# Performance work log

Measured on AMD Instinct MI355X. Metric: run time of the kernel, lower is better.

Reference implementation:

```python
import jax, jax.numpy as jnp
import numpy as np

N_NODES = 100000
N_EDGES = 1600000
NFEAT, NHID, NCLASS = 512, 256, 128
K_HOPS = 5
ALPHA = 0.1


def setup_inputs() -> dict:
    key = jax.random.key(0)
    ks = jax.random.split(key, 7)
    x = jax.random.normal(ks[0], (N_NODES, NFEAT), dtype=jnp.float32)
    edge_index = jax.random.randint(ks[1], (2, N_EDGES), 0, N_NODES, dtype=jnp.int64)
    edge_weight = jax.random.uniform(ks[2], (N_EDGES,), dtype=jnp.float32)
    # Glorot-ish scaled linear weights
    W1 = jax.random.normal(ks[3], (NFEAT, NHID), dtype=jnp.float32) * (1.0 / np.sqrt(NFEAT))
    b1 = jnp.zeros((NHID,), dtype=jnp.float32)
    W2 = jax.random.normal(ks[4], (NHID, NCLASS), dtype=jnp.float32) * (1.0 / np.sqrt(NHID))
    b2 = jnp.zeros((NCLASS,), dtype=jnp.float32)
    return {"x": x, "edge_index": edge_index, "edge_weight": edge_weight,
            "W1": W1, "b1": b1, "W2": W2, "b2": b2}


def reference(x, edge_index, edge_weight, W1, b1, W2, b2):
    # 2-layer MLP (act after first layer only; dropout p=0)
    h = jnp.maximum(x @ W1 + b1, 0.0)
    h = h @ W2 + b2  # [N, nclass]
    src = edge_index[0]
    dst = edge_index[1]
    x0 = h

    def step(carry, _):
        # gather by source, scale by edge weight, scatter-add at target
        msg = carry[src] * edge_weight[:, None]          # [E, nclass]
        agg = jax.ops.segment_sum(msg, dst, num_segments=N_NODES)
        out = (1.0 - ALPHA) * agg + ALPHA * x0           # restart mix
        return out, None

    xK, _ = jax.lax.scan(step, x0, None, length=K_HOPS)
    return jax.nn.log_softmax(xK, axis=1)
```

## Files before the change

kernel.cpp:

```cpp
#include <hip/hip_runtime.h>
#include <hip/hip_bf16.h>
#include <cstdint>
#include <cstddef>

#define N_NODES 100000
#define NFEAT 512
#define NHID 256
#define NCLASS 128
#define K_HOPS 5
#define ALPHA 0.1f

typedef __attribute__((ext_vector_type(8))) short short8v;
typedef __attribute__((ext_vector_type(4))) float f32x4;

__device__ __forceinline__ unsigned short f2bf(float f) {
    unsigned u = __builtin_bit_cast(unsigned, f);
    u += 0x7FFFu + ((u >> 16) & 1u);
    return (unsigned short)(u >> 16);
}
__device__ __forceinline__ float bflo(unsigned u) {
    return __builtin_bit_cast(float, u << 16);
}
__device__ __forceinline__ float bfhi(unsigned u) {
    return __builtin_bit_cast(float, u & 0xFFFF0000u);
}
__device__ __forceinline__ unsigned cvtpk2(float a, float b) {
    unsigned r;
    asm("v_cvt_pk_bf16_f32 %0, %1, %2" : "=v"(r) : "v"(a), "v"(b));
    return r;
}
__device__ __forceinline__ void gload_lds16(const void* g, void* l) {
    __builtin_amdgcn_global_load_lds((const __attribute__((address_space(1))) void*)g,
                                     (__attribute__((address_space(3))) void*)l, 16, 0, 0);
}


__global__ void count_kernel(const int* __restrict__ dst, int* __restrict__ counts, int E) {
    int i = blockIdx.x * blockDim.x + threadIdx.x;
    if (i < E) atomicAdd(&counts[dst[i]], 1);
}

__global__ __launch_bounds__(256) void scan_p1(const int* __restrict__ counts,
                                               int* __restrict__ partial, int n) {
    __shared__ int ws[4];
    int b = blockIdx.x, t = threadIdx.x;
    int base = b * 1024 + t * 4;
    int s = 0;
#pragma unroll
    for (int j = 0; j < 4; ++j) {
        int idx = base + j;
        if (idx < n) s += counts[idx];
    }
#pragma unroll
    for (int off = 32; off; off >>= 1) s += __shfl_xor(s, off, 64);
    if ((t & 63) == 0) ws[t >> 6] = s;
    __syncthreads();
    if (t == 0) partial[b] = ws[0] + ws[1] + ws[2] + ws[3];
}

__global__ __launch_bounds__(128) void scan_p2(int* __restrict__ partial, int nb) {
    __shared__ int s[128];
    int t = threadIdx.x;
    int v = (t < nb) ? partial[t] : 0;
    s[t] = v;
    __syncthreads();
    for (int off = 1; off < 128; off <<= 1) {
        int u = (t >= off) ? s[t - off] : 0;
        __syncthreads();
        s[t] += u;
        __syncthreads();
    }
    if (t < nb) partial[t] = (t == 0) ? 0 : s[t - 1];
}

__global__ __launch_bounds__(256) void scan_p3(const int* __restrict__ counts,
                                               const int* __restrict__ partial,
                                               int* __restrict__ row_ptr,
                                               int* __restrict__ fill, int n) {
    __shared__ int ts[256];
    int b = blockIdx.x, t = threadIdx.x;
    int base = b * 1024 + t * 4;
    int c[4];
#pragma unroll
    for (int j = 0; j < 4; ++j) {
        int idx = base + j;
        c[j] = (idx < n) ? counts[idx] : 0;
    }
    int s = c[0] + c[1] + c[2] + c[3];
    ts[t] = s;
    __syncthreads();
    for (int off = 1; off < 256; off <<= 1) {
        int v = (t >= off) ? ts[t - off] : 0;
        __syncthreads();
        ts[t] += v;
        __syncthreads();
    }
    int pre = partial[b] + ((t == 0) ? 0 : ts[t - 1]);
#pragma unroll
    for (int j = 0; j < 4; ++j) {
        int idx = base + j;
        if (idx < n) {
            row_ptr[idx] = pre;
            fill[idx] = pre;
            if (idx == n - 1) row_ptr[n] = pre + c[j];
            pre += c[j];
        }
    }
}

__global__ void scatter_kernel(const int* __restrict__ src, const int* __restrict__ dst,
                               const float* __restrict__ w, int* __restrict__ fill,
                               int2* __restrict__ epk, int E) {
    int i = blockIdx.x * blockDim.x + threadIdx.x;
    if (i < E) {
        int d = dst[i];
        int pos = atomicAdd(&fill[d], 1);
        int2 m; m.x = src[i]; m.y = __builtin_bit_cast(int, w[i]);
        epk[pos] = m;
    }
}

__global__ void wtrans_kernel(const float* __restrict__ W, unsigned short* __restrict__ Wt,
                              int K, int N) {
    int idx = blockIdx.x * blockDim.x + threadIdx.x;
    if (idx >= N * K) return;
    int n = idx / K, k = idx - n * K;
    Wt[idx] = f2bf(W[(size_t)k * N + n]);
}

template<int K, int N, int RELU, int AF32>
__global__ __launch_bounds__(256) void gemm_mfma(const void* __restrict__ Ain,
                                                 const unsigned short* __restrict__ Wt,
                                                 const float* __restrict__ bias,
                                                 unsigned short* __restrict__ Cout, int M) {
    extern __shared__ char smem[];
    constexpr int ABYTES = AF32 ? 16384 : 8192;
    constexpr int ASTEP  = AF32 ? 128 : 64;
    constexpr int NCA    = AF32 ? 4 : 2;
    char* Abase = smem;
    char* Bbase = smem + 2 * ABYTES;

    const int tid = threadIdx.x;
    const int lane = tid & 63;
    const int wv = tid >> 6;
    const int wr = wv >> 1, wc = wv & 1;
    const int brow = blockIdx.y * 128;
    const int bcol = blockIdx.x * 128;
    const float* Af = (const float*)Ain;
    const unsigned short* Ab = (const unsigned short*)Ain;

    const char* asrc[NCA];
    int aci[NCA];
#pragma unroll
    for (int c = 0; c < NCA; ++c) {
        int ci = wv + c * 4;
        aci[c] = ci;
        int ms = AF32 ? (ci & 7) : ci;
        int koff = (lane >> 4) * 8 + (AF32 ? (ci >> 3) * 4 : 0);
        int ar = brow + ms * 16 + (lane & 15); if (ar > M - 1) ar = M - 1;
        asrc[c] = AF32 ? (const char*)&Af[(size_t)ar * K + koff]
                       : (const char*)&Ab[(size_t)ar * K + koff];
    }
    const char* bsrc[2];
#pragma unroll
    for (int c = 0; c < 2; ++c) {
        int ci = wv + c * 4;
        int bc = bcol + ci * 16 + (lane & 15);
        bsrc[c] = (const char*)&Wt[(size_t)bc * K + (lane >> 4) * 8];
    }

    f32x4 acc[4][4];
#pragma unroll
    for (int m = 0; m < 4; ++m)
#pragma unroll
        for (int n = 0; n < 4; ++n) acc[m][n] = f32x4{0.f, 0.f, 0.f, 0.f};

    auto stage = [&](int buf, int step) {
        char* la = Abase + buf * ABYTES;
        char* lb = Bbase + buf * 8192;
#pragma unroll
        for (int c = 0; c < NCA; ++c)
            gload_lds16(asrc[c] + (size_t)step * ASTEP, la + aci[c] * 1024);
#pragma unroll
        for (int c = 0; c < 2; ++c)
            gload_lds16(bsrc[c] + (size_t)step * 64, lb + (wv + c * 4) * 1024);
    };

    constexpr int NSTEP = K / 32;
    int cur = 0;
    stage(0, 0);
    asm volatile("s_waitcnt vmcnt(0)" ::: "memory");
    __syncthreads();

    for (int s = 0; s < NSTEP; ++s) {
        if (s + 1 < NSTEP) stage(cur ^ 1, s + 1);

        short8v a[4], b[4];
        if constexpr (AF32) {
            const float* Asf = (const float*)(Abase + cur * ABYTES);
#pragma unroll
            for (int m = 0; m < 4; ++m) {
                int g = (wr * 4 + m) * 64 + lane;
                f32x4 lo = *(const f32x4*)&Asf[g * 4];
                f32x4 hi = *(const f32x4*)&Asf[(512 + g) * 4];
                uint4 u;
                u.x = cvtpk2(lo[0], lo[1]); u.y = cvtpk2(lo[2], lo[3]);
                u.z = cvtpk2(hi[0], hi[1]); u.w = cvtpk2(hi[2], hi[3]);
                a[m] = __builtin_bit_cast(short8v, u);
            }
        } else {
            const unsigned short* As16 = (const unsigned short*)(Abase + cur * ABYTES);
#pragma unroll
            for (int m = 0; m < 4; ++m)
                a[m] = *(const short8v*)&As16[((wr * 4 + m) * 64 + lane) * 8];
        }
        const unsigned short* Bs16 = (const unsigned short*)(Bbase + cur * 8192);
#pragma unroll
        for (int n = 0; n < 4; ++n)
            b[n] = *(const short8v*)&Bs16[((wc * 4 + n) * 64 + lane) * 8];

#pragma unroll
        for (int m = 0; m < 4; ++m)
#pragma unroll
            for (int n = 0; n < 4; ++n)
                acc[m][n] = __builtin_amdgcn_mfma_f32_16x16x32_bf16(a[m], b[n], acc[m][n], 0, 0, 0);

        asm volatile("s_waitcnt vmcnt(0)" ::: "memory");
        __syncthreads();
        cur ^= 1;
    }

#pragma unroll
    for (int n = 0; n < 4; ++n) {
        int colg = bcol + wc * 64 + n * 16 + (lane & 15);
        float bv = bias[colg];
#pragma unroll
        for (int m = 0; m < 4; ++m) {
#pragma unroll
            for (int r = 0; r < 4; ++r) {
                int rowg = brow + wr * 64 + m * 16 + (lane >> 4) * 4 + r;
                if (rowg < M) {
                    float v = acc[m][n][r] + bv;
                    if constexpr (RELU) v = fmaxf(v, 0.f);
                    Cout[(size_t)rowg * N + colg] = f2bf(v);
                }
            }
        }
    }
}

template<int FINAL>
__global__ __launch_bounds__(256) void hop_kernel(const unsigned short* __restrict__ carry,
                                                  const unsigned short* __restrict__ c0,
                                                  const int* __restrict__ rp,
                                                  const int2* __restrict__ epk,
                                                  unsigned short* __restrict__ outb,
                                                  float* __restrict__ outf, int nnodes) {
    int node = blockIdx.x * 4 + (threadIdx.x >> 6);
    if (node >= nnodes) return;
    int lane = threadIdx.x & 63;
    int e0 = rp[node], e1 = rp[node + 1];

    float a0x = 0.f, a0y = 0.f, a1x = 0.f, a1y = 0.f;
    float a2x = 0.f, a2y = 0.f, a3x = 0.f, a3y = 0.f;

    for (int eb = e0; eb < e1; eb += 64) {
        int nb = e1 - eb; if (nb > 64) nb = 64;
        int cs = 0, wvi = 0;
        if (lane < nb) {
            int2 m = epk[eb + lane];
            cs = m.x; wvi = m.y;
        }
        int j = 0;
        for (; j + 7 < nb; j += 8) {
            int s0 = __builtin_amdgcn_readlane(cs, j);
            int s1 = __builtin_amdgcn_readlane(cs, j + 1);
            int s2 = __builtin_amdgcn_readlane(cs, j + 2);
            int s3 = __builtin_amdgcn_readlane(cs, j + 3);
            int s4 = __builtin_amdgcn_readlane(cs, j + 4);
            int s5 = __builtin_amdgcn_readlane(cs, j + 5);
            int s6 = __builtin_amdgcn_readlane(cs, j + 6);
            int s7 = __builtin_amdgcn_readlane(cs, j + 7);
            float w0 = __builtin_bit_cast(float, __builtin_amdgcn_readlane(wvi, j));
            float w1 = __builtin_bit_cast(float, __builtin_amdgcn_readlane(wvi, j + 1));
            float w2 = __builtin_bit_cast(float, __builtin_amdgcn_readlane(wvi, j + 2));
            float w3 = __builtin_bit_cast(float, __builtin_amdgcn_readlane(wvi, j + 3));
            float w4 = __builtin_bit_cast(float, __builtin_amdgcn_readlane(wvi, j + 4));
            float w5 = __builtin_bit_cast(float, __builtin_amdgcn_readlane(wvi, j + 5));
            float w6 = __builtin_bit_cast(float, __builtin_amdgcn_readlane(wvi, j + 6));
            float w7 = __builtin_bit_cast(float, __builtin_amdgcn_readlane(wvi, j + 7));
            unsigned u0 = ((const unsigned*)(carry + ((size_t)s0 << 7)))[lane];
            unsigned u1 = ((const unsigned*)(carry + ((size_t)s1 << 7)))[lane];
            unsigned u2 = ((const unsigned*)(carry + ((size_t)s2 << 7)))[lane];
            unsigned u3 = ((const unsigned*)(carry + ((size_t)s3 << 7)))[lane];
            unsigned u4 = ((const unsigned*)(carry + ((size_t)s4 << 7)))[lane];
            unsigned u5 = ((const unsigned*)(carry + ((size_t)s5 << 7)))[lane];
            unsigned u6 = ((const unsigned*)(carry + ((size_t)s6 << 7)))[lane];
            unsigned u7 = ((const unsigned*)(carry + ((size_t)s7 << 7)))[lane];
            a0x = fmaf(w0, bflo(u0), a0x); a0y = fmaf(w0, bfhi(u0), a0y);
            a1x = fmaf(w1, bflo(u1), a1x); a1y = fmaf(w1, bfhi(u1), a1y);
            a2x = fmaf(w2, bflo(u2), a2x); a2y = fmaf(w2, bfhi(u2), a2y);
            a3x = fmaf(w3, bflo(u3), a3x); a3y = fmaf(w3, bfhi(u3), a3y);
            a0x = fmaf(w4, bflo(u4), a0x); a0y = fmaf(w4, bfhi(u4), a0y);
            a1x = fmaf(w5, bflo(u5), a1x); a1y = fmaf(w5, bfhi(u5), a1y);
            a2x = fmaf(w6, bflo(u6), a2x); a2y = fmaf(w6, bfhi(u6), a2y);
            a3x = fmaf(w7, bflo(u7), a3x); a3y = fmaf(w7, bfhi(u7), a3y);
        }
        for (; j + 3 < nb; j += 4) {
            int s0 = __builtin_amdgcn_readlane(cs, j);
            int s1 = __builtin_amdgcn_readlane(cs, j + 1);
            int s2 = __builtin_amdgcn_readlane(cs, j + 2);
            int s3 = __builtin_amdgcn_readlane(cs, j + 3);
            float w0 = __builtin_bit_cast(float, __builtin_amdgcn_readlane(wvi, j));
            float w1 = __builtin_bit_cast(float, __builtin_amdgcn_readlane(wvi, j + 1));
            float w2 = __builtin_bit_cast(float, __builtin_amdgcn_readlane(wvi, j + 2));
            float w3 = __builtin_bit_cast(float, __builtin_amdgcn_readlane(wvi, j + 3));
            unsigned u0 = ((const unsigned*)(carry + ((size_t)s0 << 7)))[lane];
            unsigned u1 = ((const unsigned*)(carry + ((size_t)s1 << 7)))[lane];
            unsigned u2 = ((const unsigned*)(carry + ((size_t)s2 << 7)))[lane];
            unsigned u3 = ((const unsigned*)(carry + ((size_t)s3 << 7)))[lane];
            a0x = fmaf(w0, bflo(u0), a0x); a0y = fmaf(w0, bfhi(u0), a0y);
            a1x = fmaf(w1, bflo(u1), a1x); a1y = fmaf(w1, bfhi(u1), a1y);
            a2x = fmaf(w2, bflo(u2), a2x); a2y = fmaf(w2, bfhi(u2), a2y);
            a3x = fmaf(w3, bflo(u3), a3x); a3y = fmaf(w3, bfhi(u3), a3y);
        }
        for (; j < nb; ++j) {
            int s0 = __builtin_amdgcn_readlane(cs, j);
            float w0 = __builtin_bit_cast(float, __builtin_amdgcn_readlane(wvi, j));
            unsigned u0 = ((const unsigned*)(carry + ((size_t)s0 << 7)))[lane];
            a0x = fmaf(w0, bflo(u0), a0x); a0y = fmaf(w0, bfhi(u0), a0y);
        }
    }

    unsigned ux = ((const unsigned*)(c0 + ((size_t)node << 7)))[lane];
    float vx = (1.f - ALPHA) * (a0x + a1x + a2x + a3x) + ALPHA * bflo(ux);
    float vy = (1.f - ALPHA) * (a0y + a1y + a2y + a3y) + ALPHA * bfhi(ux);

    if (FINAL) {
        float mx = fmaxf(vx, vy);
#pragma unroll
        for (int off = 32; off; off >>= 1) mx = fmaxf(mx, __shfl_xor(mx, off, 64));
        float se = __expf(vx - mx) + __expf(vy - mx);
#pragma unroll
        for (int off = 32; off; off >>= 1) se += __shfl_xor(se, off, 64);
        float l = mx + __logf(se);
        float2 o; o.x = vx - l; o.y = vy - l;
        ((float2*)(outf + ((size_t)node << 7)))[lane] = o;
    } else {
        unsigned o = (unsigned)f2bf(vx) | ((unsigned)f2bf(vy) << 16);
        ((unsigned*)(outb + ((size_t)node << 7)))[lane] = o;
    }
}


extern "C" void kernel_launch(void* const* d_in, const int* in_sizes, int n_in,
                              void* d_out, int out_size, void* d_ws, size_t ws_size,
                              hipStream_t stream) {
    const float* x   = (const float*)d_in[0];
    const int*   ei  = (const int*)d_in[1];
    const float* ew  = (const float*)d_in[2];
    const float* W1  = (const float*)d_in[3];
    const float* b1  = (const float*)d_in[4];
    const float* W2  = (const float*)d_in[5];
    const float* b2  = (const float*)d_in[6];
    float* outp = (float*)d_out;

    const int E = in_sizes[1] / 2;
    const int Nn = N_NODES;
    const int* srcv = ei;
    const int* dstv = ei + E;
    const size_t NC = (size_t)Nn * NCLASS;

    unsigned short* c0  = (unsigned short*)d_ws;
    unsigned short* A16 = c0 + NC;
    unsigned short* B16 = A16 + NC;
    unsigned short* hb  = A16;
    unsigned short* w1t = B16 + NC;
    unsigned short* w2t = w1t + NHID * NFEAT;
    int* row_ptr = (int*)(w2t + NCLASS * NHID);
    int* fill    = row_ptr + (Nn + 1);
    int* partial = fill + Nn;
    int2* epk    = (int2*)(partial + 128);

    const int NB = (Nn + 1023) / 1024;

    hipMemsetAsync(fill, 0, (size_t)Nn * sizeof(int), stream);
    count_kernel<<<(E + 255) / 256, 256, 0, stream>>>(dstv, fill, E);
    scan_p1<<<NB, 256, 0, stream>>>(fill, partial, Nn);
    scan_p2<<<1, 128, 0, stream>>>(partial, NB);
    scan_p3<<<NB, 256, 0, stream>>>(fill, partial, row_ptr, fill, Nn);
    scatter_kernel<<<(E + 255) / 256, 256, 0, stream>>>(srcv, dstv, ew, fill, epk, E);

    wtrans_kernel<<<(NHID * NFEAT + 255) / 256, 256, 0, stream>>>(W1, w1t, NFEAT, NHID);
    wtrans_kernel<<<(NCLASS * NHID + 255) / 256, 256, 0, stream>>>(W2, w2t, NHID, NCLASS);

    {
        dim3 g1(NHID / 128, (Nn + 127) / 128);
        gemm_mfma<NFEAT, NHID, 1, 1><<<g1, 256, 49152, stream>>>(x, w1t, b1, hb, Nn);
        dim3 g2(NCLASS / 128, (Nn + 127) / 128);
        gemm_mfma<NHID, NCLASS, 0, 0><<<g2, 256, 32768, stream>>>(hb, w2t, b2, c0, Nn);
    }

    int grid = (Nn + 3) / 4;
    const unsigned short* carry = c0;
    unsigned short* dsts[2] = {A16, B16};
    for (int k = 0; k < K_HOPS - 1; ++k) {
        unsigned short* o = dsts[k & 1];
        hop_kernel<0><<<grid, 256, 0, stream>>>(carry, c0, row_ptr, epk, o, nullptr, Nn);
        carry = o;
    }
    hop_kernel<1><<<grid, 256, 0, stream>>>(carry, c0, row_ptr, epk, nullptr, outp, Nn);
}
```

Baseline: 666.6 us.

## Deepen GEMM pipelines to 4-buffer prefetch and widen GEMM1 to full 256 columns

New measurement: 640.4 us. 3.9% less time.

```diff
diff --git a/kernel.cpp b/kernel.cpp
--- a/kernel.cpp
+++ b/kernel.cpp
@@ -128,45 +128,140 @@
     Wt[idx] = f2bf(W[(size_t)k * N + n]);
 }
 
-template<int K, int N, int RELU, int AF32>
-__global__ __launch_bounds__(256) void gemm_mfma(const void* __restrict__ Ain,
-                                                 const unsigned short* __restrict__ Wt,
-                                                 const float* __restrict__ bias,
-                                                 unsigned short* __restrict__ Cout, int M) {
-    extern __shared__ char smem[];
-    constexpr int ABYTES = AF32 ? 16384 : 8192;
-    constexpr int ASTEP  = AF32 ? 128 : 64;
-    constexpr int NCA    = AF32 ? 4 : 2;
-    char* Abase = smem;
-    char* Bbase = smem + 2 * ABYTES;
+__global__ __launch_bounds__(512) void gemm1_pipe(const float* __restrict__ X,
+                                                  const unsigned short* __restrict__ W1t,
+                                                  const float* __restrict__ b1,
+                                                  unsigned short* __restrict__ Hb, int M) {
+    __shared__ char smem[131072];
+    char* const Ab0 = smem;
+    char* const Bb0 = smem + 65536;
+
+    const int tid = threadIdx.x;
+    const int lane = tid & 63;
+    const int wv = tid >> 6;
+    const int wr = wv >> 2, wc = wv & 3;
+    const int brow = blockIdx.x * 128;
+
+    const char* asrc[2];
+    int adst[2];
+#pragma unroll
+    for (int c = 0; c < 2; ++c) {
+        int ar = brow + wv * 16 + (lane & 15); if (ar > M - 1) ar = M - 1;
+        int k = (lane >> 4) * 8 + c * 4;
+        asrc[c] = (const char*)&X[(size_t)ar * NFEAT + k];
+        adst[c] = (wv + c * 8) * 1024;
+    }
+    const char* bsrc[2];
+    int bdst[2];
+#pragma unroll
+    for (int c = 0; c < 2; ++c) {
+        int ci = wv + c * 8;
+        int col = ci * 16 + (lane & 15);
+        bsrc[c] = (const char*)&W1t[(size_t)col * NFEAT + (lane >> 4) * 8];
+        bdst[c] = ci * 1024;
+    }
+
+    f32x4 acc[4][4];
+#pragma unroll
+    for (int m = 0; m < 4; ++m)
+#pragma unroll
+        for (int n = 0; n < 4; ++n) acc[m][n] = f32x4{0.f, 0.f, 0.f, 0.f};
+
+    auto stage = [&](int buf, int step) {
+#pragma unroll
+        for (int c = 0; c < 2; ++c)
+            gload_lds16(asrc[c] + (size_t)step * 128, Ab0 + buf * 16384 + adst[c]);
+#pragma unroll
+        for (int c = 0; c < 2; ++c)
+            gload_lds16(bsrc[c] + (size_t)step * 64, Bb0 + buf * 16384 + bdst[c]);
+    };
+
+    constexpr int NSTEP = NFEAT / 32;
+    stage(0, 0);
+    stage(1, 1);
+
+    for (int s = 0; s < NSTEP; ++s) {
+        if (s + 2 < NSTEP) {
+            stage((s + 2) & 3, s + 2);
+            asm volatile("s_waitcnt vmcnt(8)" ::: "memory");
+        } else if (s + 1 < NSTEP) {
+            asm volatile("s_waitcnt vmcnt(4)" ::: "memory");
+        } else {
+            asm volatile("s_waitcnt vmcnt(0)" ::: "memory");
+        }
+        __builtin_amdgcn_s_barrier();
+        asm volatile("" ::: "memory");
+
+        const char* Abuf = Ab0 + (s & 3) * 16384;
+        const char* Bbuf = Bb0 + (s & 3) * 16384;
+        short8v a[4], b[4];
+#pragma unroll
+        for (int m = 0; m < 4; ++m) {
+            int g = ((wr * 4 + m) * 64 + lane) * 16;
+            f32x4 lo = *(const f32x4*)(Abuf + g);
+            f32x4 hi = *(const f32x4*)(Abuf + 8192 + g);
+            uint4 u;
+            u.x = cvtpk2(lo[0], lo[1]); u.y = cvtpk2(lo[2], lo[3]);
+            u.z = cvtpk2(hi[0], hi[1]); u.w = cvtpk2(hi[2], hi[3]);
+            a[m] = __builtin_bit_cast(short8v, u);
+        }
+#pragma unroll
+        for (int n = 0; n < 4; ++n)
+            b[n] = *(const short8v*)(Bbuf + ((wc * 4 + n) * 64 + lane) * 16);
+#pragma unroll
+        for (int m = 0; m < 4; ++m)
+#pragma unroll
+            for (int n = 0; n < 4; ++n)
+                acc[m][n] = __builtin_amdgcn_mfma_f32_16x16x32_bf16(a[m], b[n], acc[m][n], 0, 0, 0);
+
+        __builtin_amdgcn_s_barrier();
+        asm volatile("" ::: "memory");
+    }
+
+#pragma unroll
+    for (int n = 0; n < 4; ++n) {
+        int colg = wc * 64 + n * 16 + (lane & 15);
+        float bv = b1[colg];
+#pragma unroll
+        for (int m = 0; m < 4; ++m) {
+#pragma unroll
+            for (int r = 0; r < 4; ++r) {
+                int rowg = brow + wr * 64 + m * 16 + (lane >> 4) * 4 + r;
+                if (rowg < M) {
+                    float v = fmaxf(acc[m][n][r] + bv, 0.f);
+                    Hb[(size_t)rowg * NHID + colg] = f2bf(v);
+                }
+            }
+        }
+    }
+}
+
+__global__ __launch_bounds__(256) void gemm2_pipe(const unsigned short* __restrict__ Hb,
+                                                  const unsigned short* __restrict__ W2t,
+                                                  const float* __restrict__ b2,
+                                                  unsigned short* __restrict__ C0, int M) {
+    __shared__ char smem[65536];
+    char* const Ab0 = smem;
+    char* const Bb0 = smem + 32768;
 
     const int tid = threadIdx.x;
     const int lane = tid & 63;
     const int wv = tid >> 6;
     const int wr = wv >> 1, wc = wv & 1;
-    const int brow = blockIdx.y * 128;
-    const int bcol = blockIdx.x * 128;
-    const float* Af = (const float*)Ain;
-    const unsigned short* Ab = (const unsigned short*)Ain;
-
-    const char* asrc[NCA];
-    int aci[NCA];
-#pragma unroll
-    for (int c = 0; c < NCA; ++c) {
-        int ci = wv + c * 4;
-        aci[c] = ci;
-        int ms = AF32 ? (ci & 7) : ci;
-        int koff = (lane >> 4) * 8 + (AF32 ? (ci >> 3) * 4 : 0);
-        int ar = brow + ms * 16 + (lane & 15); if (ar > M - 1) ar = M - 1;
-        asrc[c] = AF32 ? (const char*)&Af[(size_t)ar * K + koff]
-                       : (const char*)&Ab[(size_t)ar * K + koff];
-    }
+    const int brow = blockIdx.x * 128;
+
+    const char* asrc[2];
     const char* bsrc[2];
+    int adst[2], bdst[2];
 #pragma unroll
     for (int c = 0; c < 2; ++c) {
         int ci = wv + c * 4;
-        int bc = bcol + ci * 16 + (lane & 15);
-        bsrc[c] = (const char*)&Wt[(size_t)bc * K + (lane >> 4) * 8];
+        int ar = brow + ci * 16 + (lane & 15); if (ar > M - 1) ar = M - 1;
+        asrc[c] = (const char*)&Hb[(size_t)ar * NHID + (lane >> 4) * 8];
+        adst[c] = ci * 1024;
+        int col = ci * 16 + (lane & 15);
+        bsrc[c] = (const char*)&W2t[(size_t)col * NHID + (lane >> 4) * 8];
+        bdst[c] = ci * 1024;
     }
 
     f32x4 acc[4][4];
@@ -176,74 +271,60 @@
         for (int n = 0; n < 4; ++n) acc[m][n] = f32x4{0.f, 0.f, 0.f, 0.f};
 
     auto stage = [&](int buf, int step) {
-        char* la = Abase + buf * ABYTES;
-        char* lb = Bbase + buf * 8192;
-#pragma unroll
-        for (int c = 0; c < NCA; ++c)
-            gload_lds16(asrc[c] + (size_t)step * ASTEP, la + aci[c] * 1024);
 #pragma unroll
         for (int c = 0; c < 2; ++c)
-            gload_lds16(bsrc[c] + (size_t)step * 64, lb + (wv + c * 4) * 1024);
+            gload_lds16(asrc[c] + (size_t)step * 64, Ab0 + buf * 8192 + adst[c]);
+#pragma unroll
+        for (int c = 0; c < 2; ++c)
+            gload_lds16(bsrc[c] + (size_t)step * 64, Bb0 + buf * 8192 + bdst[c]);
     };
 
-    constexpr int NSTEP = K / 32;
-    int cur = 0;
+    constexpr int NSTEP = NHID / 32;
     stage(0, 0);
-    asm volatile("s_waitcnt vmcnt(0)" ::: "memory");
-    __syncthreads();
+    stage(1, 1);
 
     for (int s = 0; s < NSTEP; ++s) {
-        if (s + 1 < NSTEP) stage(cur ^ 1, s + 1);
-
+        if (s + 2 < NSTEP) {
+            stage((s + 2) & 3, s + 2);
+            asm volatile("s_waitcnt vmcnt(8)" ::: "memory");
+        } else if (s + 1 < NSTEP) {
+            asm volatile("s_waitcnt vmcnt(4)" ::: "memory");
+        } else {
+            asm volatile("s_waitcnt vmcnt(0)" ::: "memory");
+        }
+        __builtin_amdgcn_s_barrier();
+        asm volatile("" ::: "memory");
+
+        const char* Abuf = Ab0 + (s & 3) * 8192;
+        const char* Bbuf = Bb0 + (s & 3) * 8192;
         short8v a[4], b[4];
-        if constexpr (AF32) {
-            const float* Asf = (const float*)(Abase + cur * ABYTES);
-#pragma unroll
-            for (int m = 0; m < 4; ++m) {
-                int g = (wr * 4 + m) * 64 + lane;
-                f32x4 lo = *(const f32x4*)&Asf[g * 4];
-                f32x4 hi = *(const f32x4*)&Asf[(512 + g) * 4];
-                uint4 u;
-                u.x = cvtpk2(lo[0], lo[1]); u.y = cvtpk2(lo[2], lo[3]);
-                u.z = cvtpk2(hi[0], hi[1]); u.w = cvtpk2(hi[2], hi[3]);
-                a[m] = __builtin_bit_cast(short8v, u);
-            }
-        } else {
-            const unsigned short* As16 = (const unsigned short*)(Abase + cur * ABYTES);
-#pragma unroll
-            for (int m = 0; m < 4; ++m)
-                a[m] = *(const short8v*)&As16[((wr * 4 + m) * 64 + lane) * 8];
-        }
-        const unsigned short* Bs16 = (const unsigned short*)(Bbase + cur * 8192);
+#pragma unroll
+        for (int m = 0; m < 4; ++m)
+            a[m] = *(const short8v*)(Abuf + ((wr * 4 + m) * 64 + lane) * 16);
 #pragma unroll
         for (int n = 0; n < 4; ++n)
-            b[n] = *(const short8v*)&Bs16[((wc * 4 + n) * 64 + lane) * 8];
-
+            b[n] = *(const short8v*)(Bbuf + ((wc * 4 + n) * 64 + lane) * 16);
 #pragma unroll
         for (int m = 0; m < 4; ++m)
 #pragma unroll
             for (int n = 0; n < 4; ++n)
                 acc[m][n] = __builtin_amdgcn_mfma_f32_16x16x32_bf16(a[m], b[n], acc[m][n], 0, 0, 0);
 
-        asm volatile("s_waitcnt vmcnt(0)" ::: "memory");
-        __syncthreads();
-        cur ^= 1;
+        __builtin_amdgcn_s_barrier();
+        asm volatile("" ::: "memory");
     }
 
 #pragma unroll
     for (int n = 0; n < 4; ++n) {
-        int colg = bcol + wc * 64 + n * 16 + (lane & 15);
-        float bv = bias[colg];
+        int colg = wc * 64 + n * 16 + (lane & 15);
+        float bv = b2[colg];
 #pragma unroll
         for (int m = 0; m < 4; ++m) {
 #pragma unroll
             for (int r = 0; r < 4; ++r) {
                 int rowg = brow + wr * 64 + m * 16 + (lane >> 4) * 4 + r;
-                if (rowg < M) {
-                    float v = acc[m][n][r] + bv;
-                    if constexpr (RELU) v = fmaxf(v, 0.f);
-                    Cout[(size_t)rowg * N + colg] = f2bf(v);
-                }
+                if (rowg < M)
+                    C0[(size_t)rowg * NCLASS + colg] = f2bf(acc[m][n][r] + bv);
             }
         }
     }
@@ -395,10 +476,9 @@
     wtrans_kernel<<<(NCLASS * NHID + 255) / 256, 256, 0, stream>>>(W2, w2t, NHID, NCLASS);
 
     {
-        dim3 g1(NHID / 128, (Nn + 127) / 128);
-        gemm_mfma<NFEAT, NHID, 1, 1><<<g1, 256, 49152, stream>>>(x, w1t, b1, hb, Nn);
-        dim3 g2(NCLASS / 128, (Nn + 127) / 128);
-        gemm_mfma<NHID, NCLASS, 0, 0><<<g2, 256, 32768, stream>>>(hb, w2t, b2, c0, Nn);
+        int gm = (Nn + 127) / 128;
+        gemm1_pipe<<<gm, 512, 0, stream>>>(x, w1t, b1, hb, Nn);
+        gemm2_pipe<<<gm, 256, 0, stream>>>(hb, w2t, b2, c0, Nn);
     }
 
     int grid = (Nn + 3) / 4;
```
